# Kernel optimization log

Hardware: AMD Instinct MI355X
Metric: run time of the kernel (lower is better)

Reference implementation:

```python
import jax, jax.numpy as jnp
import numpy as np
import math

B, T, D = 2, 2048, 1024
NH = 16
HD = D // NH


def setup_inputs() -> dict:
    key = jax.random.key(0)
    k1, k2, k3 = jax.random.split(key, 3)
    scale = 0.02
    x = jax.random.normal(k1, (B, T, D), dtype=jnp.float32)
    Wqkv = jax.random.normal(k2, (D, 3 * D), dtype=jnp.float32) * scale
    bqkv = jnp.zeros((3 * D,), dtype=jnp.float32)
    Wproj = jax.random.normal(k3, (D, D), dtype=jnp.float32) * scale
    bproj = jnp.zeros((D,), dtype=jnp.float32)
    return {"x": x, "Wqkv": Wqkv, "bqkv": bqkv, "Wproj": Wproj, "bproj": bproj}


def reference(x, Wqkv, bqkv, Wproj, bproj):
    b, t, c = x.shape
    qkv = x @ Wqkv + bqkv                      # [B,T,3D]
    q, k, v = jnp.split(qkv, 3, axis=2)
    # [B,T,NH,HD] -> [B,NH,T,HD]
    q = q.reshape(b, t, NH, HD).transpose(0, 2, 1, 3)
    k = k.reshape(b, t, NH, HD).transpose(0, 2, 1, 3)
    v = v.reshape(b, t, NH, HD).transpose(0, 2, 1, 3)
    att = jnp.einsum('bhqd,bhkd->bhqk', q, k) / math.sqrt(HD)  # [B,NH,T,T]
    causal = jnp.tril(jnp.ones((t, t), dtype=bool))
    att = jnp.where(causal, att, -jnp.inf)
    att = jax.nn.softmax(att, axis=-1)
    y = jnp.einsum('bhqk,bhkd->bhqd', att, v)  # [B,NH,T,HD]
    y = y.transpose(0, 2, 1, 3).reshape(b, t, c)
    return y @ Wproj + bproj
```

## Files before the change

kernel.cpp:

```cpp
#include <hip/hip_runtime.h>
#include <hip/hip_bf16.h>

#define B_   2
#define T_   2048
#define D_   1024
#define NH_  16
#define HD_  64
#define MROWS (B_*T_)
#define HEADELEMS (B_*NH_*T_*HD_)

#define QSCALE 0.180336880f

typedef unsigned short u16;
typedef unsigned int   u32;

typedef float f32x4  __attribute__((ext_vector_type(4)));
typedef short bf16x8 __attribute__((ext_vector_type(8)));

#define GLP(g, l) __builtin_amdgcn_global_load_lds(                         \
    (const __attribute__((address_space(1))) void*)(g),                     \
    (__attribute__((address_space(3))) void*)(l), 16, 0, 0)

struct Fc { static constexpr bool value = false; };
struct Tc { static constexpr bool value = true;  };

__device__ __forceinline__ u16 f2bf(float f) {
    u32 x = __float_as_uint(f);
    u32 r = (x + 0x7fffu + ((x >> 16) & 1u)) >> 16;
    return (u16)r;
}
__device__ __forceinline__ u32 pkbf2(float a, float b) {
    __hip_bfloat162 h = __float22bfloat162_rn(make_float2(a, b));
    union { __hip_bfloat162 h2; u32 u; } cv; cv.h2 = h; return cv.u;
}

__device__ __forceinline__ void transpose_tile(const float* in, u16* out,
                                               int K, int N, int bx, int by,
                                               int t, float (*Ts)[65])
{
    const int n0 = bx * 64;
    const int k0 = by * 64;
    #pragma unroll
    for (int pass = 0; pass < 4; pass++) {
        const int r = pass * 16 + (t >> 4);
        const int c = (t & 15) * 4;
        float4 v = *(const float4*)(in + (size_t)(k0 + r) * N + n0 + c);
        Ts[r][c] = v.x; Ts[r][c+1] = v.y; Ts[r][c+2] = v.z; Ts[r][c+3] = v.w;
    }
    __syncthreads();
    #pragma unroll
    for (int pass = 0; pass < 2; pass++) {
        const int nn = pass * 32 + (t >> 3);
        const int kk = (t & 7) * 8;
        u16 o[8];
        #pragma unroll
        for (int j = 0; j < 8; j++) o[j] = f2bf(Ts[kk + j][nn]);
        *(uint4*)(out + (size_t)(n0 + nn) * K + k0 + kk) = *(const uint4*)o;
    }
}

__global__ __launch_bounds__(256)
void prep_kernel(const float* __restrict__ x, const float* __restrict__ Wqkv,
                 u16* __restrict__ xb, u16* __restrict__ WqkvT)
{
    __shared__ float Ts[64][65];
    const int bid = blockIdx.x;
    const int t   = threadIdx.x;
    if (bid < 4096) {
        int i = bid * 256 + t;
        float4 v = ((const float4*)x)[i];
        ushort4 o;
        o.x = f2bf(v.x); o.y = f2bf(v.y); o.z = f2bf(v.z); o.w = f2bf(v.w);
        ((ushort4*)xb)[i] = o;
    } else {
        int tb = bid - 4096;
        transpose_tile(Wqkv, WqkvT, D_, 3*D_, tb % 48, tb / 48, t, Ts);
    }
}

__global__ __launch_bounds__(256)
void transpose_conv_kernel(const float* __restrict__ in, u16* __restrict__ out,
                           int K, int N)
{
    __shared__ float Ts[64][65];
    transpose_tile(in, out, K, N, blockIdx.x, blockIdx.y, threadIdx.x, Ts);
}

template <int MODE>
__global__ __launch_bounds__(256)
void gemm_mfma(const u16* __restrict__ A, const u16* __restrict__ BT,
               const float* __restrict__ bias, void* __restrict__ outv,
               int M, int N, int K)
{
    __shared__ u16 As[128][32];
    __shared__ u16 Bs[128][32];

    const int t    = threadIdx.x;
    const int wave = t >> 6;
    const int lane = t & 63;
    const int l16  = lane & 15;
    const int quad = lane >> 4;

    const int m0 = blockIdx.y * 128;
    const int n0 = blockIdx.x * 128;
    const int mb = (wave >> 1) * 64;
    const int nb = (wave & 1) * 64;

    const int r0a  = wave * 16;
    const int r0b  = 64 + wave * 16;
    const int lr_a = r0a + (lane >> 2);
    const int lr_b = r0b + (lane >> 2);
    const int sega = (((lane & 3) ^ ((lr_a >> 1) & 3))) * 8;
    const int segb = (((lane & 3) ^ ((lr_b >> 1) & 3))) * 8;

    const u16* gA0 = A  + (size_t)(m0 + lr_a) * K + sega;
    const u16* gA1 = A  + (size_t)(m0 + lr_b) * K + segb;
    const u16* gB0 = BT + (size_t)(n0 + lr_a) * K + sega;
    const u16* gB1 = BT + (size_t)(n0 + lr_b) * K + segb;

    const int fragoff = (quad ^ ((l16 >> 1) & 3)) * 8;

    f32x4 acc[4][4];
    #pragma unroll
    for (int i = 0; i < 4; i++)
        #pragma unroll
        for (int j = 0; j < 4; j++) acc[i][j] = (f32x4){0,0,0,0};

    for (int k0 = 0; k0 < K; k0 += 32) {
        __syncthreads();
        GLP(gA0 + k0, &As[r0a][0]);
        GLP(gA1 + k0, &As[r0b][0]);
        GLP(gB0 + k0, &Bs[r0a][0]);
        GLP(gB1 + k0, &Bs[r0b][0]);
        __syncthreads();

        bf16x8 af[4], bfr[4];
        #pragma unroll
        for (int i = 0; i < 4; i++)
            af[i] = *(const bf16x8*)&As[mb + i*16 + l16][fragoff];
        #pragma unroll
        for (int j = 0; j < 4; j++)
            bfr[j] = *(const bf16x8*)&Bs[nb + j*16 + l16][fragoff];

        #pragma unroll
        for (int i = 0; i < 4; i++)
            #pragma unroll
            for (int j = 0; j < 4; j++)
                acc[i][j] = __builtin_amdgcn_mfma_f32_16x16x32_bf16(
                    af[i], bfr[j], acc[i][j], 0, 0, 0);
    }

    #pragma unroll
    for (int j = 0; j < 4; j++) {
        const int n = n0 + nb + j*16 + l16;
        const float bv = bias[n];
        #pragma unroll
        for (int i = 0; i < 4; i++) {
            #pragma unroll
            for (int r = 0; r < 4; r++) {
                const int m = m0 + mb + i*16 + quad*4 + r;
                float v = acc[i][j][r] + bv;
                if (MODE == 0) {
                    ((float*)outv)[(size_t)m * N + n] = v;
                } else {
                    const int b   = m >> 11;
                    const int tt  = m & 2047;
                    const int sec = n >> 10;
                    const int dd  = n & 1023;
                    const int h   = dd >> 6;
                    const int hd  = dd & 63;
                    const size_t hbase = ((size_t)(b*NH_ + h)) * T_ * HD_;
                    size_t idx;
                    if (sec == 2)
                        idx = (size_t)2 * HEADELEMS + hbase + (size_t)hd * T_ + tt;
                    else
                        idx = (size_t)sec * HEADELEMS + hbase + (size_t)tt * HD_ + hd;
                    if (sec == 0) v *= QSCALE;
                    ((u16*)outv)[idx] = f2bf(v);
                }
            }
        }
    }
}

__global__ __launch_bounds__(256)
void attn_mfma_kernel(const u16* __restrict__ Q, const u16* __restrict__ K,
                      const u16* __restrict__ VT, u16* __restrict__ y1)
{
    __shared__ u16 Ks[2][64][72];
    __shared__ u16 Vs[2][64][72];

    const int t    = threadIdx.x;
    const int wave = t >> 6;
    const int lane = t & 63;
    const int l16  = lane & 15;
    const int quad = lane >> 4;

    const int hb = blockIdx.x;
    const int yy = blockIdx.y;
    const int qt = (yy < 8) ? (15 - yy) : (yy - 8);
    const int b  = hb >> 4;
    const int h  = hb & 15;
    const size_t base = (size_t)hb * T_ * HD_;

    const int qw0 = qt * 128 + wave * 32;

    bf16x8 qf[2][2];
    #pragma unroll
    for (int mi = 0; mi < 2; mi++) {
        const u16* qp = Q + base + (size_t)(qw0 + mi*16 + l16) * HD_ + quad * 8;
        qf[mi][0] = *(const bf16x8*)(qp);
        qf[mi][1] = *(const bf16x8*)(qp + 32);
    }

    bf16x8 onesf;
    #pragma unroll
    for (int i = 0; i < 8; i++) onesf[i] = (short)0x3F80;

    f32x4 o[2][4];
    #pragma unroll
    for (int mi = 0; mi < 2; mi++)
        #pragma unroll
        for (int d = 0; d < 4; d++) o[mi][d] = (f32x4){0,0,0,0};
    f32x4 accl[2] = {(f32x4){0,0,0,0}, (f32x4){0,0,0,0}};

    const int nsteps = 2 * qt + 2;
    const int fullw  = qw0 >> 6;

    const int srow = t >> 3;
    const int scol = (t & 7) * 8;

    const int srcA  = l16 + ((quad & 1) << 5);
    const int srcB  = srcA + 16;
    const bool selhi = (quad >> 1) != 0;

    uint4 kr0, kr1, vr0, vr1;
    {
        const u16* kp = K + base + (size_t)srow * HD_ + scol;
        kr0 = *(const uint4*)kp;
        kr1 = *(const uint4*)(kp + 32 * HD_);
        const u16* vp = VT + base + (size_t)srow * T_ + scol;
        vr0 = *(const uint4*)vp;
        vr1 = *(const uint4*)(vp + 32 * T_);
        *(uint4*)&Ks[0][srow][scol]      = kr0;
        *(uint4*)&Ks[0][srow + 32][scol] = kr1;
        *(uint4*)&Vs[0][srow][scol]      = vr0;
        *(uint4*)&Vs[0][srow + 32][scol] = vr1;
    }
    __syncthreads();

    auto compute_tile = [&](int cur, int k0, auto mc) {
        constexpr bool MASKED = decltype(mc)::value;
        f32x4 st[2][4];
        #pragma unroll
        for (int j = 0; j < 4; j++) {
            bf16x8 kf0 = *(const bf16x8*)&Ks[cur][j*16 + l16][quad * 8];
            bf16x8 kf1 = *(const bf16x8*)&Ks[cur][j*16 + l16][32 + quad * 8];
            #pragma unroll
            for (int mi = 0; mi < 2; mi++) {
                f32x4 z = {0,0,0,0};
                z = __builtin_amdgcn_mfma_f32_16x16x32_bf16(kf0, qf[mi][0], z, 0, 0, 0);
                st[mi][j] = __builtin_amdgcn_mfma_f32_16x16x32_bf16(kf1, qf[mi][1], z, 0, 0, 0);
            }
        }

        u32 p01[2][4], p23[2][4];
        #pragma unroll
        for (int mi = 0; mi < 2; mi++) {
            const int qi = qw0 + mi*16 + l16;
            #pragma unroll
            for (int j = 0; j < 4; j++) {
                const int kb = k0 + j*16 + quad*4;
                float e0 = __builtin_amdgcn_exp2f(st[mi][j][0]);
                float e1 = __builtin_amdgcn_exp2f(st[mi][j][1]);
                float e2 = __builtin_amdgcn_exp2f(st[mi][j][2]);
                float e3 = __builtin_amdgcn_exp2f(st[mi][j][3]);
                if (MASKED) {
                    if (kb + 0 > qi) e0 = 0.f;
                    if (kb + 1 > qi) e1 = 0.f;
                    if (kb + 2 > qi) e2 = 0.f;
                    if (kb + 3 > qi) e3 = 0.f;
                }
                p01[mi][j] = pkbf2(e0, e1);
                p23[mi][j] = pkbf2(e2, e3);
            }
        }

        #pragma unroll
        for (int mi = 0; mi < 2; mi++) {
            bf16x8 pf[2];
            #pragma unroll
            for (int c = 0; c < 2; c++) {
                u32 t0, t1, r01, r23, r45, r67;
                t0 = (u32)__shfl((int)p01[mi][2*c],   srcA);
                t1 = (u32)__shfl((int)p01[mi][2*c+1], srcA);
                r01 = selhi ? t1 : t0;
                t0 = (u32)__shfl((int)p23[mi][2*c],   srcA);
                t1 = (u32)__shfl((int)p23[mi][2*c+1], srcA);
                r23 = selhi ? t1 : t0;
                t0 = (u32)__shfl((int)p01[mi][2*c],   srcB);
                t1 = (u32)__shfl((int)p01[mi][2*c+1], srcB);
                r45 = selhi ? t1 : t0;
                t0 = (u32)__shfl((int)p23[mi][2*c],   srcB);
                t1 = (u32)__shfl((int)p23[mi][2*c+1], srcB);
                r67 = selhi ? t1 : t0;
                union { u32 u[4]; bf16x8 v; } pk;
                pk.u[0] = r01; pk.u[1] = r23; pk.u[2] = r45; pk.u[3] = r67;
                pf[c] = pk.v;
            }
            accl[mi] = __builtin_amdgcn_mfma_f32_16x16x32_bf16(pf[0], onesf, accl[mi], 0, 0, 0);
            accl[mi] = __builtin_amdgcn_mfma_f32_16x16x32_bf16(pf[1], onesf, accl[mi], 0, 0, 0);
            #pragma unroll
            for (int d = 0; d < 4; d++) {
                bf16x8 v0 = *(const bf16x8*)&Vs[cur][d*16 + l16][quad * 8];
                bf16x8 v1 = *(const bf16x8*)&Vs[cur][d*16 + l16][32 + quad * 8];
                o[mi][d] = __builtin_amdgcn_mfma_f32_16x16x32_bf16(pf[0], v0, o[mi][d], 0, 0, 0);
                o[mi][d] = __builtin_amdgcn_mfma_f32_16x16x32_bf16(pf[1], v1, o[mi][d], 0, 0, 0);
            }
        }
    };

    for (int kt = 0; kt < nsteps; kt++) {
        const int cur = kt & 1;
        const int k0  = kt * 64;
        const bool have_next = (kt + 1 < nsteps);

        if (have_next) {
            const u16* kp = K + base + (size_t)(k0 + 64 + srow) * HD_ + scol;
            kr0 = *(const uint4*)kp;
            kr1 = *(const uint4*)(kp + 32 * HD_);
            const u16* vp = VT + base + (size_t)srow * T_ + k0 + 64 + scol;
            vr0 = *(const uint4*)vp;
            vr1 = *(const uint4*)(vp + 32 * T_);
        }

        if (kt < fullw)        compute_tile(cur, k0, Fc{});
        else if (kt == fullw)  compute_tile(cur, k0, Tc{});

        if (have_next) {
            const int nxt = cur ^ 1;
            *(uint4*)&Ks[nxt][srow][scol]      = kr0;
            *(uint4*)&Ks[nxt][srow + 32][scol] = kr1;
            *(uint4*)&Vs[nxt][srow][scol]      = vr0;
            *(uint4*)&Vs[nxt][srow + 32][scol] = vr1;
            __syncthreads();
        }
    }

    #pragma unroll
    for (int mi = 0; mi < 2; mi++) {
        #pragma unroll
        for (int r = 0; r < 4; r++) {
            const float inv = 1.f / accl[mi][r];
            const int qi = qw0 + mi*16 + quad*4 + r;
            u16* yp = y1 + ((size_t)(b * T_ + qi)) * D_ + h * HD_ + l16;
            yp[0]  = f2bf(o[mi][0][r] * inv);
            yp[16] = f2bf(o[mi][1][r] * inv);
            yp[32] = f2bf(o[mi][2][r] * inv);
            yp[48] = f2bf(o[mi][3][r] * inv);
        }
    }
}

extern "C" void kernel_launch(void* const* d_in, const int* in_sizes, int n_in,
                              void* d_out, int out_size, void* d_ws, size_t ws_size,
                              hipStream_t stream)
{
    const float* x     = (const float*)d_in[0];
    const float* Wqkv  = (const float*)d_in[1];
    const float* bqkv  = (const float*)d_in[2];
    const float* Wproj = (const float*)d_in[3];
    const float* bproj = (const float*)d_in[4];

    u16* scratch = (u16*)d_out;
    u16* xb      = scratch;
    u16* WqkvT   = scratch + (size_t)MROWS * D_;

    u16* qkv = (u16*)d_ws;
    u16* Qp  = qkv;
    u16* Kp  = qkv + (size_t)HEADELEMS;
    u16* Vtp = qkv + (size_t)2 * HEADELEMS;
    u16* WprojT = Kp;

    const bool big_ws = ws_size >= (size_t)4 * HEADELEMS * sizeof(u16);
    u16* y1b = big_ws ? qkv + (size_t)3 * HEADELEMS : scratch;
    u16* y1g = big_ws ? y1b : Vtp;

    prep_kernel<<<4096 + 768, 256, 0, stream>>>(x, Wqkv, xb, WqkvT);

    gemm_mfma<1><<<dim3(3*D_/128, MROWS/128), 256, 0, stream>>>(
        xb, WqkvT, bqkv, (void*)qkv, MROWS, 3*D_, D_);

    attn_mfma_kernel<<<dim3(NH_*B_, T_/128), 256, 0, stream>>>(Qp, Kp, Vtp, y1b);

    transpose_conv_kernel<<<dim3(D_/64, D_/64), 256, 0, stream>>>(
        Wproj, WprojT, D_, D_);

    if (!big_ws)
        (void)hipMemcpyAsync(y1g, y1b, (size_t)MROWS * D_ * sizeof(u16),
                             hipMemcpyDeviceToDevice, stream);

    gemm_mfma<0><<<dim3(D_/128, MROWS/128), 256, 0, stream>>>(
        y1g, WprojT, bproj, d_out, MROWS, D_, D_);
}
```

Before: 210.5 us.

## Halve attention query tile to 64 rows and fold Wproj transpose into prep

The attention kernel now gives each block 64 query rows instead of 128, one 16-row MFMA tile per wave, and launches twice as many blocks in a reordered heavy/light pattern. This is meant to improve load balance and occupancy across the causal triangle. In exchange, each K/V tile loaded into shared memory is reused by half as many query rows. When the workspace is large enough, the Wproj transpose-convert moves into the prep kernel so one launch is removed.

Measured after the change: 197.5 us. 1.07x faster.

```diff
diff --git a/kernel.cpp b/kernel.cpp
--- a/kernel.cpp
+++ b/kernel.cpp
@@ -61,7 +61,8 @@
 
 __global__ __launch_bounds__(256)
 void prep_kernel(const float* __restrict__ x, const float* __restrict__ Wqkv,
-                 u16* __restrict__ xb, u16* __restrict__ WqkvT)
+                 const float* __restrict__ Wproj, u16* __restrict__ xb,
+                 u16* __restrict__ WqkvT, u16* __restrict__ WprojT)
 {
     __shared__ float Ts[64][65];
     const int bid = blockIdx.x;
@@ -72,9 +73,12 @@
         ushort4 o;
         o.x = f2bf(v.x); o.y = f2bf(v.y); o.z = f2bf(v.z); o.w = f2bf(v.w);
         ((ushort4*)xb)[i] = o;
-    } else {
+    } else if (bid < 4096 + 768) {
         int tb = bid - 4096;
         transpose_tile(Wqkv, WqkvT, D_, 3*D_, tb % 48, tb / 48, t, Ts);
+    } else {
+        int tb = bid - 4864;
+        transpose_tile(Wproj, WprojT, D_, D_, tb % 16, tb / 16, t, Ts);
     }
 }
 
@@ -198,34 +202,32 @@
 
     const int hb = blockIdx.x;
     const int yy = blockIdx.y;
-    const int qt = (yy < 8) ? (15 - yy) : (yy - 8);
+    const int a  = yy & 7, g = yy >> 3;
+    const int qt = (g == 0) ? 31 - a : (g == 1) ? 16 + a
+                 : (g == 2) ? 15 - a : a;
     const int b  = hb >> 4;
     const int h  = hb & 15;
     const size_t base = (size_t)hb * T_ * HD_;
 
-    const int qw0 = qt * 128 + wave * 32;
-
-    bf16x8 qf[2][2];
-    #pragma unroll
-    for (int mi = 0; mi < 2; mi++) {
-        const u16* qp = Q + base + (size_t)(qw0 + mi*16 + l16) * HD_ + quad * 8;
-        qf[mi][0] = *(const bf16x8*)(qp);
-        qf[mi][1] = *(const bf16x8*)(qp + 32);
+    const int qw0 = qt * 64 + wave * 16;
+
+    bf16x8 qf[2];
+    {
+        const u16* qp = Q + base + (size_t)(qw0 + l16) * HD_ + quad * 8;
+        qf[0] = *(const bf16x8*)(qp);
+        qf[1] = *(const bf16x8*)(qp + 32);
     }
 
     bf16x8 onesf;
     #pragma unroll
     for (int i = 0; i < 8; i++) onesf[i] = (short)0x3F80;
 
-    f32x4 o[2][4];
-    #pragma unroll
-    for (int mi = 0; mi < 2; mi++)
-        #pragma unroll
-        for (int d = 0; d < 4; d++) o[mi][d] = (f32x4){0,0,0,0};
-    f32x4 accl[2] = {(f32x4){0,0,0,0}, (f32x4){0,0,0,0}};
-
-    const int nsteps = 2 * qt + 2;
-    const int fullw  = qw0 >> 6;
+    f32x4 o[4];
+    #pragma unroll
+    for (int d = 0; d < 4; d++) o[d] = (f32x4){0,0,0,0};
+    f32x4 accl = (f32x4){0,0,0,0};
+
+    const int nsteps = qt + 1;
 
     const int srow = t >> 3;
     const int scol = (t & 7) * 8;
@@ -251,72 +253,63 @@
 
     auto compute_tile = [&](int cur, int k0, auto mc) {
         constexpr bool MASKED = decltype(mc)::value;
-        f32x4 st[2][4];
+        f32x4 st[4];
         #pragma unroll
         for (int j = 0; j < 4; j++) {
             bf16x8 kf0 = *(const bf16x8*)&Ks[cur][j*16 + l16][quad * 8];
             bf16x8 kf1 = *(const bf16x8*)&Ks[cur][j*16 + l16][32 + quad * 8];
-            #pragma unroll
-            for (int mi = 0; mi < 2; mi++) {
-                f32x4 z = {0,0,0,0};
-                z = __builtin_amdgcn_mfma_f32_16x16x32_bf16(kf0, qf[mi][0], z, 0, 0, 0);
-                st[mi][j] = __builtin_amdgcn_mfma_f32_16x16x32_bf16(kf1, qf[mi][1], z, 0, 0, 0);
+            f32x4 z = {0,0,0,0};
+            z = __builtin_amdgcn_mfma_f32_16x16x32_bf16(kf0, qf[0], z, 0, 0, 0);
+            st[j] = __builtin_amdgcn_mfma_f32_16x16x32_bf16(kf1, qf[1], z, 0, 0, 0);
+        }
+
+        u32 p01[4], p23[4];
+        const int qi = qw0 + l16;
+        #pragma unroll
+        for (int j = 0; j < 4; j++) {
+            const int kb = k0 + j*16 + quad*4;
+            float e0 = __builtin_amdgcn_exp2f(st[j][0]);
+            float e1 = __builtin_amdgcn_exp2f(st[j][1]);
+            float e2 = __builtin_amdgcn_exp2f(st[j][2]);
+            float e3 = __builtin_amdgcn_exp2f(st[j][3]);
+            if (MASKED) {
+                if (kb + 0 > qi) e0 = 0.f;
+                if (kb + 1 > qi) e1 = 0.f;
+                if (kb + 2 > qi) e2 = 0.f;
+                if (kb + 3 > qi) e3 = 0.f;
             }
-        }
-
-        u32 p01[2][4], p23[2][4];
-        #pragma unroll
-        for (int mi = 0; mi < 2; mi++) {
-            const int qi = qw0 + mi*16 + l16;
-            #pragma unroll
-            for (int j = 0; j < 4; j++) {
-                const int kb = k0 + j*16 + quad*4;
-                float e0 = __builtin_amdgcn_exp2f(st[mi][j][0]);
-                float e1 = __builtin_amdgcn_exp2f(st[mi][j][1]);
-                float e2 = __builtin_amdgcn_exp2f(st[mi][j][2]);
-                float e3 = __builtin_amdgcn_exp2f(st[mi][j][3]);
-                if (MASKED) {
-                    if (kb + 0 > qi) e0 = 0.f;
-                    if (kb + 1 > qi) e1 = 0.f;
-                    if (kb + 2 > qi) e2 = 0.f;
-                    if (kb + 3 > qi) e3 = 0.f;
-                }
-                p01[mi][j] = pkbf2(e0, e1);
-                p23[mi][j] = pkbf2(e2, e3);
-            }
-        }
-
-        #pragma unroll
-        for (int mi = 0; mi < 2; mi++) {
-            bf16x8 pf[2];
-            #pragma unroll
-            for (int c = 0; c < 2; c++) {
-                u32 t0, t1, r01, r23, r45, r67;
-                t0 = (u32)__shfl((int)p01[mi][2*c],   srcA);
-                t1 = (u32)__shfl((int)p01[mi][2*c+1], srcA);
-                r01 = selhi ? t1 : t0;
-                t0 = (u32)__shfl((int)p23[mi][2*c],   srcA);
-                t1 = (u32)__shfl((int)p23[mi][2*c+1], srcA);
-                r23 = selhi ? t1 : t0;
-                t0 = (u32)__shfl((int)p01[mi][2*c],   srcB);
-                t1 = (u32)__shfl((int)p01[mi][2*c+1], srcB);
-                r45 = selhi ? t1 : t0;
-                t0 = (u32)__shfl((int)p23[mi][2*c],   srcB);
-                t1 = (u32)__shfl((int)p23[mi][2*c+1], srcB);
-                r67 = selhi ? t1 : t0;
-                union { u32 u[4]; bf16x8 v; } pk;
-                pk.u[0] = r01; pk.u[1] = r23; pk.u[2] = r45; pk.u[3] = r67;
-                pf[c] = pk.v;
-            }
-            accl[mi] = __builtin_amdgcn_mfma_f32_16x16x32_bf16(pf[0], onesf, accl[mi], 0, 0, 0);
-            accl[mi] = __builtin_amdgcn_mfma_f32_16x16x32_bf16(pf[1], onesf, accl[mi], 0, 0, 0);
-            #pragma unroll
-            for (int d = 0; d < 4; d++) {
-                bf16x8 v0 = *(const bf16x8*)&Vs[cur][d*16 + l16][quad * 8];
-                bf16x8 v1 = *(const bf16x8*)&Vs[cur][d*16 + l16][32 + quad * 8];
-                o[mi][d] = __builtin_amdgcn_mfma_f32_16x16x32_bf16(pf[0], v0, o[mi][d], 0, 0, 0);
-                o[mi][d] = __builtin_amdgcn_mfma_f32_16x16x32_bf16(pf[1], v1, o[mi][d], 0, 0, 0);
-            }
+            p01[j] = pkbf2(e0, e1);
+            p23[j] = pkbf2(e2, e3);
+        }
+
+        bf16x8 pf[2];
+        #pragma unroll
+        for (int c = 0; c < 2; c++) {
+            u32 t0, t1, r01, r23, r45, r67;
+            t0 = (u32)__shfl((int)p01[2*c],   srcA);
+            t1 = (u32)__shfl((int)p01[2*c+1], srcA);
+            r01 = selhi ? t1 : t0;
+            t0 = (u32)__shfl((int)p23[2*c],   srcA);
+            t1 = (u32)__shfl((int)p23[2*c+1], srcA);
+            r23 = selhi ? t1 : t0;
+            t0 = (u32)__shfl((int)p01[2*c],   srcB);
+            t1 = (u32)__shfl((int)p01[2*c+1], srcB);
+            r45 = selhi ? t1 : t0;
+            t0 = (u32)__shfl((int)p23[2*c],   srcB);
+            t1 = (u32)__shfl((int)p23[2*c+1], srcB);
+            r67 = selhi ? t1 : t0;
+            union { u32 u[4]; bf16x8 v; } pk;
+            pk.u[0] = r01; pk.u[1] = r23; pk.u[2] = r45; pk.u[3] = r67;
+            pf[c] = pk.v;
+        }
+        accl = __builtin_amdgcn_mfma_f32_16x16x32_bf16(pf[0], onesf, accl, 0, 0, 0);
+        accl = __builtin_amdgcn_mfma_f32_16x16x32_bf16(pf[1], onesf, accl, 0, 0, 0);
+        #pragma unroll
+        for (int d = 0; d < 4; d++) {
+            bf16x8 v0 = *(const bf16x8*)&Vs[cur][d*16 + l16][quad * 8];
+            bf16x8 v1 = *(const bf16x8*)&Vs[cur][d*16 + l16][32 + quad * 8];
+            o[d] = __builtin_amdgcn_mfma_f32_16x16x32_bf16(pf[0], v0, o[d], 0, 0, 0);
+            o[d] = __builtin_amdgcn_mfma_f32_16x16x32_bf16(pf[1], v1, o[d], 0, 0, 0);
         }
     };
 
@@ -334,8 +327,8 @@
             vr1 = *(const uint4*)(vp + 32 * T_);
         }
 
-        if (kt < fullw)        compute_tile(cur, k0, Fc{});
-        else if (kt == fullw)  compute_tile(cur, k0, Tc{});
+        if (kt < qt) compute_tile(cur, k0, Fc{});
+        else         compute_tile(cur, k0, Tc{});
 
         if (have_next) {
             const int nxt = cur ^ 1;
@@ -348,17 +341,14 @@
     }
 
     #pragma unroll
-    for (int mi = 0; mi < 2; mi++) {
-        #pragma unroll
-        for (int r = 0; r < 4; r++) {
-            const float inv = 1.f / accl[mi][r];
-            const int qi = qw0 + mi*16 + quad*4 + r;
-            u16* yp = y1 + ((size_t)(b * T_ + qi)) * D_ + h * HD_ + l16;
-            yp[0]  = f2bf(o[mi][0][r] * inv);
-            yp[16] = f2bf(o[mi][1][r] * inv);
-            yp[32] = f2bf(o[mi][2][r] * inv);
-            yp[48] = f2bf(o[mi][3][r] * inv);
-        }
+    for (int r = 0; r < 4; r++) {
+        const float inv = 1.f / accl[r];
+        const int qi = qw0 + quad*4 + r;
+        u16* yp = y1 + ((size_t)(b * T_ + qi)) * D_ + h * HD_ + l16;
+        yp[0]  = f2bf(o[0][r] * inv);
+        yp[16] = f2bf(o[1][r] * inv);
+        yp[32] = f2bf(o[2][r] * inv);
+        yp[48] = f2bf(o[3][r] * inv);
     }
 }
 
@@ -376,28 +366,35 @@
     u16* xb      = scratch;
     u16* WqkvT   = scratch + (size_t)MROWS * D_;
 
+    const size_t Y1E = (size_t)MROWS * D_;
+    const size_t WPE = (size_t)D_ * D_;
+
     u16* qkv = (u16*)d_ws;
     u16* Qp  = qkv;
     u16* Kp  = qkv + (size_t)HEADELEMS;
     u16* Vtp = qkv + (size_t)2 * HEADELEMS;
-    u16* WprojT = Kp;
-
-    const bool big_ws = ws_size >= (size_t)4 * HEADELEMS * sizeof(u16);
-    u16* y1b = big_ws ? qkv + (size_t)3 * HEADELEMS : scratch;
-    u16* y1g = big_ws ? y1b : Vtp;
-
-    prep_kernel<<<4096 + 768, 256, 0, stream>>>(x, Wqkv, xb, WqkvT);
+
+    const bool huge = ws_size >= ((size_t)3 * HEADELEMS + Y1E + WPE) * 2;
+    const bool big  = ws_size >= ((size_t)3 * HEADELEMS + Y1E) * 2;
+
+    u16* y1b    = big ? qkv + (size_t)3 * HEADELEMS : scratch;
+    u16* y1g    = big ? y1b : Vtp;
+    u16* WprojT = huge ? qkv + (size_t)3 * HEADELEMS + Y1E : Kp;
+
+    prep_kernel<<<huge ? 5120 : 4864, 256, 0, stream>>>(
+        x, Wqkv, Wproj, xb, WqkvT, WprojT);
 
     gemm_mfma<1><<<dim3(3*D_/128, MROWS/128), 256, 0, stream>>>(
         xb, WqkvT, bqkv, (void*)qkv, MROWS, 3*D_, D_);
 
-    attn_mfma_kernel<<<dim3(NH_*B_, T_/128), 256, 0, stream>>>(Qp, Kp, Vtp, y1b);
-
-    transpose_conv_kernel<<<dim3(D_/64, D_/64), 256, 0, stream>>>(
-        Wproj, WprojT, D_, D_);
-
-    if (!big_ws)
-        (void)hipMemcpyAsync(y1g, y1b, (size_t)MROWS * D_ * sizeof(u16),
+    attn_mfma_kernel<<<dim3(NH_*B_, T_/64), 256, 0, stream>>>(Qp, Kp, Vtp, y1b);
+
+    if (!huge)
+        transpose_conv_kernel<<<dim3(D_/64, D_/64), 256, 0, stream>>>(
+            Wproj, WprojT, D_, D_);
+
+    if (!big)
+        (void)hipMemcpyAsync(y1g, y1b, Y1E * sizeof(u16),
                              hipMemcpyDeviceToDevice, stream);
 
     gemm_mfma<0><<<dim3(D_/128, MROWS/128), 256, 0, stream>>>(
```
